# Kernel optimization log

Hardware: AMD Instinct MI355X
Metric: run time of the kernel (lower is better)

Reference implementation:

```python
import jax, jax.numpy as jnp
import numpy as np

N_T, D_MODEL, RANK, BATCH = 64, 1024, 8, 4096
THRESHOLD = 0.0  # jumprelu threshold (forward default)


def setup_inputs() -> dict:
    key = jax.random.key(0)
    k_x, k_v, k_u, k_e = jax.random.split(key, 4)
    scale = (1.0 / (D_MODEL * RANK)) ** 0.25
    x = jax.random.normal(k_x, (BATCH, D_MODEL), dtype=jnp.float32)
    V = jax.random.normal(k_v, (N_T, RANK, D_MODEL), dtype=jnp.float32) * scale
    U = jax.random.normal(k_u, (N_T, D_MODEL, RANK), dtype=jnp.float32) * scale
    encoder = jax.random.normal(k_e, (N_T, D_MODEL), dtype=jnp.float32)
    encoder = encoder / jnp.linalg.norm(encoder, axis=1, keepdims=True)
    bias = -jnp.ones((N_T,), dtype=jnp.float32)  # init_constant(bias, -1.0)
    return {"x": x, "V": V, "U": U, "encoder": encoder, "bias": bias}


def jumprelu(x, threshold=THRESHOLD):
    # forward: hard threshold x * 1[x > threshold]
    return x * (x > threshold).astype(x.dtype)


def reference(x, V, U, encoder, bias):
    # pre_acts: (batch, n)
    pre_acts = x @ encoder.T - bias
    gate = jumprelu(pre_acts)  # activation_fn='jumprelu', threshold=0.0
    # Vx: (n, batch, rank)
    Vx = jnp.einsum('nrd,bd->nbr', V, x)
    # UVx: (n, batch, d) -- the large intermediate a fused kernel would avoid
    UVx = jnp.einsum('ndr,nbr->nbd', U, Vx)
    # gated sum over transforms: (batch, d)
    output = jnp.einsum('nbd,bn->bd', UVx, gate)
    u_norms = jnp.linalg.norm(U.reshape(U.shape[0], -1), axis=1)
    v_norms = jnp.linalg.norm(V.reshape(V.shape[0], -1), axis=1)
    frobenius_norms = u_norms * v_norms / (D_MODEL * RANK) ** 0.5
    return output, gate, frobenius_norms
```

## Files before the change

kernel.cpp:

```cpp
#include <hip/hip_runtime.h>
#include <math.h>

#define BATCHN 4096
#define DMODEL 1024
#define NT 64
#define RANK 8
#define K2 512

typedef __attribute__((ext_vector_type(8))) short bf16x8;
typedef __attribute__((ext_vector_type(4))) float f32x4;

__device__ __forceinline__ void async16(void* lds, const void* g) {
    __builtin_amdgcn_global_load_lds(
        (const __attribute__((address_space(1))) void*)g,
        (__attribute__((address_space(3))) void*)lds, 16, 0, 0);
}

__device__ __forceinline__ short f2bf(float f) {
    unsigned u = __builtin_bit_cast(unsigned, f);
    u += 0x7fffu + ((u >> 16) & 1u);
    return (short)(u >> 16);
}

__global__ __launch_bounds__(256) void convert_kernel(
    const float* __restrict__ x, const float* __restrict__ enc,
    const float* __restrict__ V, const float* __restrict__ U,
    unsigned short* __restrict__ xb, unsigned short* __restrict__ Wb,
    unsigned short* __restrict__ Ub,
    float* __restrict__ su_part, float* __restrict__ sv_part)
{
    const int b = blockIdx.x, t = threadIdx.x;
    float s = 0.f;
    float* psum = nullptr;

    if (b < 512) {
        const size_t base = (size_t)b * 8192;
        #pragma unroll
        for (int it = 0; it < 4; ++it) {
            const size_t e = base + it * 2048 + t * 8;
            float4 v0 = *(const float4*)(x + e);
            float4 v1 = *(const float4*)(x + e + 4);
            bf16x8 o;
            o[0]=f2bf(v0.x); o[1]=f2bf(v0.y); o[2]=f2bf(v0.z); o[3]=f2bf(v0.w);
            o[4]=f2bf(v1.x); o[5]=f2bf(v1.y); o[6]=f2bf(v1.z); o[7]=f2bf(v1.w);
            *(bf16x8*)(xb + e) = o;
        }
    } else if (b < 584) {
        const size_t base = (size_t)(b - 512) * 8192;
        const bool isV = (b >= 520);
        if (isV) psum = sv_part + (b - 520);
        #pragma unroll
        for (int it = 0; it < 4; ++it) {
            const size_t e = base + it * 2048 + t * 8;
            const int row = (int)(e >> 10), col = (int)(e & 1023);
            const float* src = (row < 64)
                ? enc + (size_t)row * 1024 + col
                : V + (size_t)(row - 64) * 1024 + col;
            float4 v0 = *(const float4*)src;
            float4 v1 = *(const float4*)(src + 4);
            bf16x8 o;
            o[0]=f2bf(v0.x); o[1]=f2bf(v0.y); o[2]=f2bf(v0.z); o[3]=f2bf(v0.w);
            o[4]=f2bf(v1.x); o[5]=f2bf(v1.y); o[6]=f2bf(v1.z); o[7]=f2bf(v1.w);
            *(bf16x8*)(Wb + e) = o;
            if (isV)
                s += v0.x*v0.x + v0.y*v0.y + v0.z*v0.z + v0.w*v0.w
                   + v1.x*v1.x + v1.y*v1.y + v1.z*v1.z + v1.w*v1.w;
        }
    } else {
        const int n = b - 584;
        psum = su_part + n;
        const size_t base = (size_t)n * 8192;
        #pragma unroll
        for (int it = 0; it < 4; ++it) {
            const size_t e = base + it * 2048 + t * 8;
            float4 v0 = *(const float4*)(U + e);
            float4 v1 = *(const float4*)(U + e + 4);
            bf16x8 o;
            o[0]=f2bf(v0.x); o[1]=f2bf(v0.y); o[2]=f2bf(v0.z); o[3]=f2bf(v0.w);
            o[4]=f2bf(v1.x); o[5]=f2bf(v1.y); o[6]=f2bf(v1.z); o[7]=f2bf(v1.w);
            *(bf16x8*)(Ub + e) = o;
            s += v0.x*v0.x + v0.y*v0.y + v0.z*v0.z + v0.w*v0.w
               + v1.x*v1.x + v1.y*v1.y + v1.z*v1.z + v1.w*v1.w;
        }
    }

    if (psum) {
        #pragma unroll
        for (int off = 32; off; off >>= 1) s += __shfl_down(s, off);
        __shared__ float red[4];
        if ((t & 63) == 0) red[t >> 6] = s;
        __syncthreads();
        if (t == 0) *psum = red[0] + red[1] + red[2] + red[3];
    }
}

__global__ __launch_bounds__(256) void gatevx_kernel(
    const unsigned short* __restrict__ A, const unsigned short* __restrict__ Bm,
    const float* __restrict__ bias,
    float* __restrict__ gate_out, unsigned short* __restrict__ vx_out)
{
    constexpr int BK = 64, KDIM = DMODEL, NIT = KDIM / BK;
    __shared__ unsigned short As[2][64 * BK];
    __shared__ unsigned short Bs[2][64 * BK];
    const int t = threadIdx.x;
    const int wave = t >> 6, lane = t & 63;
    const int bm = blockIdx.y, bn = blockIdx.x;
    const int wm = wave & 1, wn = wave >> 1;
    const int lrow = lane >> 3, lchunk = lane & 7;
    const int l15 = lane & 15, lq = lane >> 4;

    f32x4 acc[2][2] = {};
    const size_t Abase = (size_t)bm * 64 * KDIM;
    const size_t Bbase = (size_t)bn * 64 * KDIM;

    auto STAGE = [&](int buf, int k0) {
        #pragma unroll
        for (int c = 0; c < 2; ++c) {
            const int row = (wave * 2 + c) * 8 + lrow;
            const int chunk = lchunk ^ lrow;
            async16(&As[buf][(wave * 2 + c) * 512],
                    A + Abase + (size_t)row * KDIM + k0 + chunk * 8);
            async16(&Bs[buf][(wave * 2 + c) * 512],
                    Bm + Bbase + (size_t)row * KDIM + k0 + chunk * 8);
        }
    };
    auto COMPUTE = [&](int buf) {
        #pragma unroll
        for (int s = 0; s < 2; ++s) {
            bf16x8 af[2], bfr[2];
            const int kc = s * 4 + lq;
            #pragma unroll
            for (int i = 0; i < 2; ++i) {
                const int m = wm * 32 + i * 16 + l15;
                af[i] = *(const bf16x8*)&As[buf][m * BK + ((kc ^ (m & 7)) * 8)];
            }
            #pragma unroll
            for (int j = 0; j < 2; ++j) {
                const int n = wn * 32 + j * 16 + l15;
                bfr[j] = *(const bf16x8*)&Bs[buf][n * BK + ((kc ^ (n & 7)) * 8)];
            }
            #pragma unroll
            for (int i = 0; i < 2; ++i)
                #pragma unroll
                for (int j = 0; j < 2; ++j)
                    acc[i][j] = __builtin_amdgcn_mfma_f32_16x16x32_bf16(
                        af[i], bfr[j], acc[i][j], 0, 0, 0);
        }
    };

    STAGE(0, 0);
    __syncthreads();
    int cur = 0;
    for (int kt = 0; kt < NIT - 1; ++kt) {
        STAGE(cur ^ 1, (kt + 1) * BK);
        COMPUTE(cur);
        __syncthreads();
        cur ^= 1;
    }
    COMPUTE(cur);
    __syncthreads();

    if (bn == 0) {
        float* Cs = (float*)&As[0][0];
        #pragma unroll
        for (int i = 0; i < 2; ++i) {
            const int rowb = wm * 32 + i * 16 + lq * 4;
            #pragma unroll
            for (int j = 0; j < 2; ++j) {
                const int col = wn * 32 + j * 16 + l15;
                const float bz = bias[col];
                #pragma unroll
                for (int r = 0; r < 4; ++r) {
                    const float p = acc[i][j][r] - bz;
                    Cs[(rowb + r) * 64 + col] = p > 0.f ? p : 0.f;
                }
            }
        }
        __syncthreads();
        #pragma unroll
        for (int p = 0; p < 4; ++p) {
            const int row = p * 16 + (t >> 4);
            const int col = (t & 15) * 4;
            *(f32x4*)&gate_out[(size_t)(bm * 64 + row) * NT + col] =
                *(const f32x4*)&Cs[row * 64 + col];
        }
    } else {
        unsigned short* Cs16 = &As[0][0];
        #pragma unroll
        for (int i = 0; i < 2; ++i) {
            const int rowb = wm * 32 + i * 16 + lq * 4;
            #pragma unroll
            for (int j = 0; j < 2; ++j) {
                const int col = wn * 32 + j * 16 + l15;
                #pragma unroll
                for (int r = 0; r < 4; ++r)
                    Cs16[(rowb + r) * 64 + col] = (unsigned short)f2bf(acc[i][j][r]);
            }
        }
        __syncthreads();
        #pragma unroll
        for (int p = 0; p < 2; ++p) {
            const int row = p * 32 + (t >> 3);
            const int chunk = t & 7;
            *(bf16x8*)&vx_out[(size_t)(bm * 64 + row) * K2 + (bn - 1) * 64 + chunk * 8] =
                *(const bf16x8*)&Cs16[row * 64 + chunk * 8];
        }
    }
}

__global__ __launch_bounds__(256) void out_kernel(
    const unsigned short* __restrict__ vx, const float* __restrict__ gate,
    const unsigned short* __restrict__ Ub, float* __restrict__ out,
    const float* __restrict__ su_part, const float* __restrict__ sv_part,
    float* __restrict__ fro)
{
    constexpr int BK = 64, KDIM = K2, NIT = KDIM / BK;
    __shared__ unsigned short As[2][64 * BK];
    __shared__ unsigned short Bs[2][8 * 2 * 64 * 8];
    const int t = threadIdx.x;
    const int wave = t >> 6, lane = t & 63;
    const int bm = blockIdx.y, bn = blockIdx.x;
    const int wm = wave & 1, wn = wave >> 1;
    const int lrow = lane >> 3, lchunk = lane & 7;
    const int l15 = lane & 15, lq = lane >> 4;

    f32x4 acc[2][4] = {};

    auto LOADA = [&](int k0, bf16x8* v, float* g) {
        #pragma unroll
        for (int c = 0; c < 2; ++c) {
            const int row = (wave * 2 + c) * 8 + lrow;
            const int grow = bm * 64 + row;
            const int chunk = lchunk ^ lrow;
            v[c] = *(const bf16x8*)(vx + (size_t)grow * K2 + k0 + chunk * 8);
            g[c] = gate[(size_t)grow * NT + (k0 >> 3) + chunk];
        }
    };
    auto WRITEA = [&](int buf, const bf16x8* v, const float* g) {
        #pragma unroll
        for (int c = 0; c < 2; ++c) {
            bf16x8 o;
            #pragma unroll
            for (int e = 0; e < 8; ++e) {
                const float f = __builtin_bit_cast(float,
                    ((unsigned)(unsigned short)v[c][e]) << 16);
                o[e] = (short)(__builtin_bit_cast(unsigned, f * g[c]) >> 16);
            }
            *(bf16x8*)&As[buf][(wave * 2 + c) * 512 + lane * 8] = o;
        }
    };
    auto STAGEB = [&](int buf, int k0) {
        #pragma unroll
        for (int c = 0; c < 4; ++c) {
            const int n_local = wave * 2 + (c >> 1);
            const int dblk = c & 1;
            const int n_glob = (k0 >> 3) + n_local;
            async16(&Bs[buf][(n_local * 2 + dblk) * 512],
                    Ub + (size_t)n_glob * (DMODEL * RANK)
                       + (size_t)(bn * 128 + dblk * 64 + lane) * RANK);
        }
    };
    auto COMPUTE = [&](int buf) {
        #pragma unroll
        for (int s = 0; s < 2; ++s) {
            bf16x8 af[2], bfr[4];
            const int kc = s * 4 + lq;
            #pragma unroll
            for (int i = 0; i < 2; ++i) {
                const int m = wm * 32 + i * 16 + l15;
                af[i] = *(const bf16x8*)&As[buf][m * BK + ((kc ^ (m & 7)) * 8)];
            }
            #pragma unroll
            for (int j = 0; j < 4; ++j) {
                const int cl = wn * 64 + j * 16 + l15;
                bfr[j] = *(const bf16x8*)&Bs[buf][((kc * 2 + (cl >> 6)) * 64 + (cl & 63)) * 8];
            }
            #pragma unroll
            for (int i = 0; i < 2; ++i)
                #pragma unroll
                for (int j = 0; j < 4; ++j)
                    acc[i][j] = __builtin_amdgcn_mfma_f32_16x16x32_bf16(
                        af[i], bfr[j], acc[i][j], 0, 0, 0);
        }
    };

    {
        bf16x8 v[2]; float g[2];
        LOADA(0, v, g);
        STAGEB(0, 0);
        WRITEA(0, v, g);
    }
    __syncthreads();
    int cur = 0;
    for (int kt = 0; kt < NIT - 1; ++kt) {
        bf16x8 v[2]; float g[2];
        LOADA((kt + 1) * BK, v, g);
        STAGEB(cur ^ 1, (kt + 1) * BK);
        COMPUTE(cur);
        WRITEA(cur ^ 1, v, g);
        __syncthreads();
        cur ^= 1;
    }
    COMPUTE(cur);
    __syncthreads();

    float* Cs = (float*)&Bs[0][0];
    #pragma unroll
    for (int i = 0; i < 2; ++i) {
        const int rowb = wm * 32 + i * 16 + lq * 4;
        #pragma unroll
        for (int j = 0; j < 4; ++j) {
            const int col = wn * 64 + j * 16 + l15;
            #pragma unroll
            for (int r = 0; r < 4; ++r)
                Cs[(rowb + r) * 128 + col] = acc[i][j][r];
        }
    }
    __syncthreads();
    #pragma unroll
    for (int p = 0; p < 8; ++p) {
        const int row = p * 8 + (t >> 5);
        const int col = (t & 31) * 4;
        *(f32x4*)&out[(size_t)(bm * 64 + row) * DMODEL + bn * 128 + col] =
            *(const f32x4*)&Cs[row * 128 + col];
    }

    if (bn == 0 && bm == 0 && t < NT) {
        fro[t] = sqrtf(su_part[t]) * sqrtf(sv_part[t]) / sqrtf((float)(DMODEL * RANK));
    }
}

extern "C" void kernel_launch(void* const* d_in, const int* in_sizes, int n_in,
                              void* d_out, int out_size, void* d_ws, size_t ws_size,
                              hipStream_t stream) {
    const float* x    = (const float*)d_in[0];
    const float* V    = (const float*)d_in[1];
    const float* U    = (const float*)d_in[2];
    const float* enc  = (const float*)d_in[3];
    const float* bias = (const float*)d_in[4];

    float* out  = (float*)d_out;
    float* gate = out + (size_t)BATCHN * DMODEL;
    float* fro  = gate + (size_t)BATCHN * NT;

    char* ws = (char*)d_ws;
    unsigned short* xb = (unsigned short*)ws;
    unsigned short* Wb = (unsigned short*)(ws + 8388608);
    unsigned short* Ub = (unsigned short*)(ws + 9568256);
    unsigned short* vx = (unsigned short*)(ws + 10616832);
    float* su_part     = (float*)(ws + 14811136);
    float* sv_part     = (float*)(ws + 14812160);

    convert_kernel<<<648, 256, 0, stream>>>(x, enc, V, U, xb, Wb, Ub, su_part, sv_part);
    gatevx_kernel<<<dim3(9, 64), 256, 0, stream>>>(xb, Wb, bias, gate, vx);
    out_kernel<<<dim3(8, 64), 256, 0, stream>>>(vx, gate, Ub, out, su_part, sv_part, fro);
}
```

Baseline: 110.4 us.

## Fuse fp32-to-bf16 conversion into gate/Vx GEMM and drop convert kernel

Removes the separate conversion kernel. The gate/Vx GEMM now loads fp32 x, encoder and V directly, converts them to bf16 in registers and writes them to LDS, with register double-buffering in place of async global-to-LDS copies. U conversion and its norm run in an extra column of blocks, and the V norm partials are computed inside the GEMM blocks for bm==0. This saves one launch and the bf16 round-trip of x through global memory. In exchange each block reads x at twice the byte width, and x is now re-read in fp32 by all nine column blocks.

```diff
diff --git a/kernel.cpp b/kernel.cpp
--- a/kernel.cpp
+++ b/kernel.cpp
@@ -22,106 +22,83 @@
     return (short)(u >> 16);
 }
 
-__global__ __launch_bounds__(256) void convert_kernel(
+__device__ __forceinline__ bf16x8 cvt8(const float4 a, const float4 b) {
+    bf16x8 o;
+    o[0]=f2bf(a.x); o[1]=f2bf(a.y); o[2]=f2bf(a.z); o[3]=f2bf(a.w);
+    o[4]=f2bf(b.x); o[5]=f2bf(b.y); o[6]=f2bf(b.z); o[7]=f2bf(b.w);
+    return o;
+}
+
+__global__ __launch_bounds__(256) void gatevx_kernel(
     const float* __restrict__ x, const float* __restrict__ enc,
     const float* __restrict__ V, const float* __restrict__ U,
-    unsigned short* __restrict__ xb, unsigned short* __restrict__ Wb,
+    const float* __restrict__ bias,
+    float* __restrict__ gate_out, unsigned short* __restrict__ vx_out,
     unsigned short* __restrict__ Ub,
     float* __restrict__ su_part, float* __restrict__ sv_part)
 {
-    const int b = blockIdx.x, t = threadIdx.x;
-    float s = 0.f;
-    float* psum = nullptr;
-
-    if (b < 512) {
-        const size_t base = (size_t)b * 8192;
-        #pragma unroll
-        for (int it = 0; it < 4; ++it) {
-            const size_t e = base + it * 2048 + t * 8;
-            float4 v0 = *(const float4*)(x + e);
-            float4 v1 = *(const float4*)(x + e + 4);
-            bf16x8 o;
-            o[0]=f2bf(v0.x); o[1]=f2bf(v0.y); o[2]=f2bf(v0.z); o[3]=f2bf(v0.w);
-            o[4]=f2bf(v1.x); o[5]=f2bf(v1.y); o[6]=f2bf(v1.z); o[7]=f2bf(v1.w);
-            *(bf16x8*)(xb + e) = o;
-        }
-    } else if (b < 584) {
-        const size_t base = (size_t)(b - 512) * 8192;
-        const bool isV = (b >= 520);
-        if (isV) psum = sv_part + (b - 520);
-        #pragma unroll
-        for (int it = 0; it < 4; ++it) {
-            const size_t e = base + it * 2048 + t * 8;
-            const int row = (int)(e >> 10), col = (int)(e & 1023);
-            const float* src = (row < 64)
-                ? enc + (size_t)row * 1024 + col
-                : V + (size_t)(row - 64) * 1024 + col;
-            float4 v0 = *(const float4*)src;
-            float4 v1 = *(const float4*)(src + 4);
-            bf16x8 o;
-            o[0]=f2bf(v0.x); o[1]=f2bf(v0.y); o[2]=f2bf(v0.z); o[3]=f2bf(v0.w);
-            o[4]=f2bf(v1.x); o[5]=f2bf(v1.y); o[6]=f2bf(v1.z); o[7]=f2bf(v1.w);
-            *(bf16x8*)(Wb + e) = o;
-            if (isV)
-                s += v0.x*v0.x + v0.y*v0.y + v0.z*v0.z + v0.w*v0.w
-                   + v1.x*v1.x + v1.y*v1.y + v1.z*v1.z + v1.w*v1.w;
-        }
-    } else {
-        const int n = b - 584;
-        psum = su_part + n;
+    __shared__ unsigned short As[2][4096];
+    __shared__ unsigned short Bs[2][4096];
+    __shared__ float red[4];
+    const int t = threadIdx.x;
+    const int bn = blockIdx.x, bm = blockIdx.y;
+    const int wave = t >> 6, lane = t & 63;
+
+    if (bn == 9) {
+        const int n = bm;
         const size_t base = (size_t)n * 8192;
+        float s = 0.f;
         #pragma unroll
         for (int it = 0; it < 4; ++it) {
             const size_t e = base + it * 2048 + t * 8;
             float4 v0 = *(const float4*)(U + e);
             float4 v1 = *(const float4*)(U + e + 4);
-            bf16x8 o;
-            o[0]=f2bf(v0.x); o[1]=f2bf(v0.y); o[2]=f2bf(v0.z); o[3]=f2bf(v0.w);
-            o[4]=f2bf(v1.x); o[5]=f2bf(v1.y); o[6]=f2bf(v1.z); o[7]=f2bf(v1.w);
-            *(bf16x8*)(Ub + e) = o;
+            *(bf16x8*)(Ub + e) = cvt8(v0, v1);
             s += v0.x*v0.x + v0.y*v0.y + v0.z*v0.z + v0.w*v0.w
                + v1.x*v1.x + v1.y*v1.y + v1.z*v1.z + v1.w*v1.w;
         }
-    }
-
-    if (psum) {
         #pragma unroll
         for (int off = 32; off; off >>= 1) s += __shfl_down(s, off);
-        __shared__ float red[4];
         if ((t & 63) == 0) red[t >> 6] = s;
         __syncthreads();
-        if (t == 0) *psum = red[0] + red[1] + red[2] + red[3];
-    }
-}
-
-__global__ __launch_bounds__(256) void gatevx_kernel(
-    const unsigned short* __restrict__ A, const unsigned short* __restrict__ Bm,
-    const float* __restrict__ bias,
-    float* __restrict__ gate_out, unsigned short* __restrict__ vx_out)
-{
+        if (t == 0) su_part[n] = red[0] + red[1] + red[2] + red[3];
+        return;
+    }
+
     constexpr int BK = 64, KDIM = DMODEL, NIT = KDIM / BK;
-    __shared__ unsigned short As[2][64 * BK];
-    __shared__ unsigned short Bs[2][64 * BK];
-    const int t = threadIdx.x;
-    const int wave = t >> 6, lane = t & 63;
-    const int bm = blockIdx.y, bn = blockIdx.x;
     const int wm = wave & 1, wn = wave >> 1;
     const int lrow = lane >> 3, lchunk = lane & 7;
     const int l15 = lane & 15, lq = lane >> 4;
 
     f32x4 acc[2][2] = {};
-    const size_t Abase = (size_t)bm * 64 * KDIM;
-    const size_t Bbase = (size_t)bn * 64 * KDIM;
-
-    auto STAGE = [&](int buf, int k0) {
+    const size_t Arow0 = (size_t)bm * 64;
+    const float* Bbase = (bn == 0) ? enc : V + (size_t)(bn - 1) * 64 * DMODEL;
+    const bool doSV = (bn >= 1) && (bm == 0);
+    float sv[2] = {0.f, 0.f};
+
+    auto LOADAB = [&](int k0, float4* a, float4* b) {
         #pragma unroll
         for (int c = 0; c < 2; ++c) {
             const int row = (wave * 2 + c) * 8 + lrow;
             const int chunk = lchunk ^ lrow;
-            async16(&As[buf][(wave * 2 + c) * 512],
-                    A + Abase + (size_t)row * KDIM + k0 + chunk * 8);
-            async16(&Bs[buf][(wave * 2 + c) * 512],
-                    Bm + Bbase + (size_t)row * KDIM + k0 + chunk * 8);
+            const float* ax = x + (Arow0 + row) * DMODEL + k0 + chunk * 8;
+            a[c*2]   = *(const float4*)ax;
+            a[c*2+1] = *(const float4*)(ax + 4);
+            const float* bx = Bbase + (size_t)row * DMODEL + k0 + chunk * 8;
+            b[c*2]   = *(const float4*)bx;
+            b[c*2+1] = *(const float4*)(bx + 4);
+        }
+    };
+    auto WRITEAB = [&](int buf, const float4* a, const float4* b) {
+        #pragma unroll
+        for (int c = 0; c < 2; ++c) {
+            *(bf16x8*)&As[buf][(wave * 2 + c) * 512 + lane * 8] = cvt8(a[c*2], a[c*2+1]);
+            *(bf16x8*)&Bs[buf][(wave * 2 + c) * 512 + lane * 8] = cvt8(b[c*2], b[c*2+1]);
+            if (doSV) {
+                const float4 b0 = b[c*2], b1 = b[c*2+1];
+                sv[c] += b0.x*b0.x + b0.y*b0.y + b0.z*b0.z + b0.w*b0.w
+                       + b1.x*b1.x + b1.y*b1.y + b1.z*b1.z + b1.w*b1.w;
+            }
         }
     };
     auto COMPUTE = [&](int buf) {
@@ -148,16 +125,32 @@
         }
     };
 
-    STAGE(0, 0);
+    {
+        float4 a[4], b[4];
+        LOADAB(0, a, b);
+        WRITEAB(0, a, b);
+    }
     __syncthreads();
     int cur = 0;
     for (int kt = 0; kt < NIT - 1; ++kt) {
-        STAGE(cur ^ 1, (kt + 1) * BK);
+        float4 a[4], b[4];
+        LOADAB((kt + 1) * BK, a, b);
         COMPUTE(cur);
+        WRITEAB(cur ^ 1, a, b);
         __syncthreads();
         cur ^= 1;
     }
     COMPUTE(cur);
+
+    if (doSV) {
+        #pragma unroll
+        for (int c = 0; c < 2; ++c) {
+            float s = sv[c];
+            #pragma unroll
+            for (int off = 32; off; off >>= 1) s += __shfl_down(s, off);
+            if (lane == 0) sv_part[(bn - 1) * 8 + wave * 2 + c] = s;
+        }
+    }
     __syncthreads();
 
     if (bn == 0) {
@@ -215,8 +208,8 @@
     float* __restrict__ fro)
 {
     constexpr int BK = 64, KDIM = K2, NIT = KDIM / BK;
-    __shared__ unsigned short As[2][64 * BK];
-    __shared__ unsigned short Bs[2][8 * 2 * 64 * 8];
+    __shared__ unsigned short As[2][4096];
+    __shared__ unsigned short Bs[2][8192];
     const int t = threadIdx.x;
     const int wave = t >> 6, lane = t & 63;
     const int bm = blockIdx.y, bn = blockIdx.x;
@@ -344,14 +337,13 @@
     float* fro  = gate + (size_t)BATCHN * NT;
 
     char* ws = (char*)d_ws;
-    unsigned short* xb = (unsigned short*)ws;
-    unsigned short* Wb = (unsigned short*)(ws + 8388608);
-    unsigned short* Ub = (unsigned short*)(ws + 9568256);
-    unsigned short* vx = (unsigned short*)(ws + 10616832);
-    float* su_part     = (float*)(ws + 14811136);
-    float* sv_part     = (float*)(ws + 14812160);
-
-    convert_kernel<<<648, 256, 0, stream>>>(x, enc, V, U, xb, Wb, Ub, su_part, sv_part);
-    gatevx_kernel<<<dim3(9, 64), 256, 0, stream>>>(xb, Wb, bias, gate, vx);
-    out_kernel<<<dim3(8, 64), 256, 0, stream>>>(vx, gate, Ub, out, su_part, sv_part, fro);
-}
+    unsigned short* Ub = (unsigned short*)ws;
+    unsigned short* vx = (unsigned short*)(ws + 1048576);
+    float* su_part     = (float*)(ws + 5242880);
+    float* sv_part     = (float*)(ws + 5244928);
+
+    gatevx_kernel<<<dim3(10, 64), 256, 0, stream>>>(
+        x, enc, V, U, bias, gate, vx, Ub, su_part, sv_part);
+    out_kernel<<<dim3(8, 64), 256, 0, stream>>>(
+        vx, gate, Ub, out, su_part, sv_part, fro);
+}
```

Result: no change. 111.2 us (+0.8%).
